# Optimization experiments

Hardware: AMD Instinct MI355X
Metric: run time of the kernel (lower is better)

The kernel has to match this reference:

```python
import jax, jax.numpy as jnp
import numpy as np

B, C, Hh, Ww = 64, 128, 28, 28   # batch, channels, subband H, subband W (H/2, W/2 of input)
NB, BS = 4, 32                    # num_blocks, block_size (C = NB*BS)
ORI = 6                           # DTCWT orientation subbands


def setup_inputs() -> dict:
    key = jax.random.key(0)
    ks = jax.random.split(key, 7)
    return {
        "xl": jax.random.normal(ks[0], (B, C, Hh, Ww), jnp.float32),
        "xh": jax.random.normal(ks[1], (B, C, ORI, Hh, Ww, 2), jnp.float32),
        "w_ll": jax.random.normal(ks[2], (C, Hh, Ww), jnp.float32) * 0.02,
        "w1": jax.random.normal(ks[3], (2, NB, BS, BS), jnp.float32) * 0.02,
        "w2": jax.random.normal(ks[4], (2, NB, BS, BS), jnp.float32) * 0.02,
        "b1": jax.random.normal(ks[5], (2, NB, BS), jnp.float32) * 0.02,
        "b2": jax.random.normal(ks[6], (2, NB, BS), jnp.float32) * 0.02,
    }


def _mul(x, w):
    # block-diagonal matmul: x [..., nb, bs_in], w [nb, bs_in, bs_out]
    return jnp.einsum('...bd,bdk->...bk', x, w)


def reference(xl, xh, w_ll, w1, w2, b1, b2):
    # lowpass: elementwise weighting (broadcast over batch)
    xl_out = xl * w_ll

    b, c = xh.shape[0], xh.shape[1]
    # (B,C,6,H,W,2) -> (2,B,6,H,W,C) -> (2,B,6,H,W,NB,BS)
    x = jnp.transpose(xh, (5, 0, 2, 3, 4, 1))
    x = x.reshape(2, b, ORI, xh.shape[3], xh.shape[4], NB, BS)
    xr, xi = x[0], x[1]

    # complex block-diagonal layer 1 + ReLU
    r1 = jax.nn.relu(_mul(xr, w1[0]) - _mul(xi, w1[1]) + b1[0])
    i1 = jax.nn.relu(_mul(xr, w1[1]) + _mul(xi, w1[0]) + b1[1])
    # complex block-diagonal layer 2 (linear)
    r2 = _mul(r1, w2[0]) - _mul(i1, w2[1]) + b2[0]
    i2 = _mul(r1, w2[1]) + _mul(i1, w2[0]) + b2[1]

    # stack real/imag last, merge blocks back to C, restore (B,C,6,H,W,2)
    out = jnp.stack([r2, i2], axis=-1)                               # (B,6,H,W,NB,BS,2)
    out = out.reshape(b, ORI, xh.shape[3], xh.shape[4], NB * BS, 2)  # (B,6,H,W,C,2)
    xh_out = jnp.transpose(out, (0, 4, 1, 2, 3, 5))                  # (B,C,6,H,W,2)
    # softshrink lambd == 0.0 -> identity (the torch code skips it)
    return xl_out, xh_out
```

## Files before the change

### kernel.cpp

```cpp
#include <hip/hip_runtime.h>

typedef __bf16 bf16x8 __attribute__((ext_vector_type(8)));
typedef float  f32x4  __attribute__((ext_vector_type(4)));


static __device__ __forceinline__ unsigned short bf16bits(float f) {
  __bf16 h = (__bf16)f;
  return __builtin_bit_cast(unsigned short, h);
}

__global__ void prep_weights(const float* __restrict__ w1, const float* __restrict__ w2,
                             unsigned short* __restrict__ wg) {
  const int e = blockIdx.x * 256 + threadIdx.x;
  const int nb    = e >> 13;
  const int layer = (e >> 12) & 1;
  const int n = (e >> 6) & 63;
  const int k = e & 63;
  const float* w = layer ? w2 : w1;
  const int kk = k & 31, nn = n & 31;
  float v;
  if (n < 32) {
    v = (k < 32) ?  w[((0 * 4 + nb) * 32 + kk) * 32 + nn]
                 : -w[((1 * 4 + nb) * 32 + kk) * 32 + nn];
  } else {
    v = (k < 32) ?  w[((1 * 4 + nb) * 32 + kk) * 32 + nn]
                 :  w[((0 * 4 + nb) * 32 + kk) * 32 + nn];
  }
  wg[e] = bf16bits(v);
}

__global__ void ll_kernel(const float* __restrict__ xl, const float* __restrict__ wll,
                          float* __restrict__ out) {
  const int i = blockIdx.x * 256 + threadIdx.x;
  const float4 x = reinterpret_cast<const float4*>(xl)[i];
  const float4 w = reinterpret_cast<const float4*>(wll)[i % 25088];
  float4 o;
  o.x = x.x * w.x; o.y = x.y * w.y; o.z = x.z * w.z; o.w = x.w * w.w;
  reinterpret_cast<float4*>(out)[i] = o;
}

__global__ __launch_bounds__(256, 3)
void xh_kernel(const float* __restrict__ xh, const unsigned short* __restrict__ wg,
               const float* __restrict__ b1, const float* __restrict__ b2,
               float* __restrict__ oxh) {
  __shared__ __align__(16) unsigned short Xs[256 * 64];
  __shared__ __align__(16) unsigned short Ws[2 * 64 * 64];
  __shared__ __align__(16) float Bs[128];

  const int t = threadIdx.x;
  const int bi = blockIdx.x;
  const int mt  = bi % 196;
  const int snb = bi / 196;
  const int ori = snb >> 2;
  const int nb  = snb & 3;
  const int p0 = mt << 8;

  if (t < 128) {
    const int layer = t >> 6, n = t & 63;
    const float* bsrc = layer ? b2 : b1;
    Bs[t] = bsrc[((n >> 5) * 4 + nb) * 32 + (n & 31)];
  }

  {
    const unsigned short* wgn = wg + nb * 8192;
#pragma unroll
    for (int it = 0; it < 4; ++it) {
      const int idx = it * 256 + t;
      const int layer = idx >> 9;
      const int n = (idx >> 3) & 63;
      const int g = idx & 7;
      const uint4 v = *reinterpret_cast<const uint4*>(wgn + layer * 4096 + n * 64 + g * 8);
      char* dst = reinterpret_cast<char*>(Ws) + layer * 8192 + n * 128 + ((g ^ ((n >> 1) & 7)) * 16);
      *reinterpret_cast<uint4*>(dst) = v;
    }
  }

  {
    const float* xb = xh + (size_t)(nb * 32) * 9408 + ori * 1568;
#pragma unroll
    for (int it = 0; it < 8; ++it) {
      const int idx = it * 256 + t;
      const int c = (idx >> 7) * 2;
      const int p = (idx & 127) * 2;
      const int P = p0 + p;
      const int bb = P / 784;
      const int hw = P - bb * 784;
      const float* src = xb + (size_t)bb * 1204224 + c * 9408 + hw * 2;
      const float4 vA = *reinterpret_cast<const float4*>(src);
      const float4 vB = *reinterpret_cast<const float4*>(src + 9408);
      const int g0 = c >> 3;
      const int off = (c & 7) * 2;
      const int s0 = (p >> 1) & 7;
      char* base = reinterpret_cast<char*>(Xs);
      *reinterpret_cast<unsigned int*>(base + p * 128 + ((g0 ^ s0) * 16) + off) =
          (unsigned int)bf16bits(vA.x) | ((unsigned int)bf16bits(vB.x) << 16);
      *reinterpret_cast<unsigned int*>(base + p * 128 + (((g0 + 4) ^ s0) * 16) + off) =
          (unsigned int)bf16bits(vA.y) | ((unsigned int)bf16bits(vB.y) << 16);
      *reinterpret_cast<unsigned int*>(base + (p + 1) * 128 + ((g0 ^ s0) * 16) + off) =
          (unsigned int)bf16bits(vA.z) | ((unsigned int)bf16bits(vB.z) << 16);
      *reinterpret_cast<unsigned int*>(base + (p + 1) * 128 + (((g0 + 4) ^ s0) * 16) + off) =
          (unsigned int)bf16bits(vA.w) | ((unsigned int)bf16bits(vB.w) << 16);
    }
  }
  __syncthreads();

  const int lane = t & 63;
  const int wv = t >> 6;
  const int lr = lane & 15;
  const int lg = lane >> 4;

  f32x4 acc[4][4];
#pragma unroll
  for (int mi = 0; mi < 4; ++mi)
#pragma unroll
    for (int ni = 0; ni < 4; ++ni)
      acc[mi][ni] = (f32x4){0.f, 0.f, 0.f, 0.f};

#pragma unroll
  for (int ks = 0; ks < 2; ++ks) {
    bf16x8 wf[4], xf[4];
#pragma unroll
    for (int mi = 0; mi < 4; ++mi) {
      const int n = mi * 16 + lr;
      wf[mi] = *reinterpret_cast<const bf16x8*>(reinterpret_cast<const char*>(Ws)
                 + n * 128 + (((ks * 4 + lg) ^ ((n >> 1) & 7)) * 16));
    }
#pragma unroll
    for (int ni = 0; ni < 4; ++ni) {
      const int p = wv * 64 + ni * 16 + lr;
      xf[ni] = *reinterpret_cast<const bf16x8*>(reinterpret_cast<const char*>(Xs)
                 + p * 128 + (((ks * 4 + lg) ^ ((p >> 1) & 7)) * 16));
    }
#pragma unroll
    for (int mi = 0; mi < 4; ++mi)
#pragma unroll
      for (int ni = 0; ni < 4; ++ni)
        acc[mi][ni] = __builtin_amdgcn_mfma_f32_16x16x32_bf16(wf[mi], xf[ni], acc[mi][ni], 0, 0, 0);
  }

#pragma unroll
  for (int mi = 0; mi < 4; ++mi) {
    const f32x4 bv = *reinterpret_cast<const f32x4*>(&Bs[mi * 16 + lg * 4]);
    const int gH = mi * 2 + (lg >> 1);
    const int offH = (lg & 1) * 8;
#pragma unroll
    for (int ni = 0; ni < 4; ++ni) {
      const int p = wv * 64 + ni * 16 + lr;
      const float h0 = fmaxf(acc[mi][ni][0] + bv[0], 0.f);
      const float h1 = fmaxf(acc[mi][ni][1] + bv[1], 0.f);
      const float h2 = fmaxf(acc[mi][ni][2] + bv[2], 0.f);
      const float h3 = fmaxf(acc[mi][ni][3] + bv[3], 0.f);
      uint2 u;
      u.x = (unsigned int)bf16bits(h0) | ((unsigned int)bf16bits(h1) << 16);
      u.y = (unsigned int)bf16bits(h2) | ((unsigned int)bf16bits(h3) << 16);
      char* dst = reinterpret_cast<char*>(Xs) + p * 128 + ((gH ^ ((p >> 1) & 7)) * 16) + offH;
      *reinterpret_cast<uint2*>(dst) = u;
    }
  }
  __syncthreads();

  f32x4 acc2[4][4];
#pragma unroll
  for (int mi = 0; mi < 4; ++mi)
#pragma unroll
    for (int ni = 0; ni < 4; ++ni)
      acc2[mi][ni] = (f32x4){0.f, 0.f, 0.f, 0.f};

#pragma unroll
  for (int ks = 0; ks < 2; ++ks) {
    bf16x8 wf[4], hf[4];
#pragma unroll
    for (int mi = 0; mi < 4; ++mi) {
      const int n = mi * 16 + lr;
      wf[mi] = *reinterpret_cast<const bf16x8*>(reinterpret_cast<const char*>(Ws)
                 + 8192 + n * 128 + (((ks * 4 + lg) ^ ((n >> 1) & 7)) * 16));
    }
#pragma unroll
    for (int ni = 0; ni < 4; ++ni) {
      const int p = wv * 64 + ni * 16 + lr;
      hf[ni] = *reinterpret_cast<const bf16x8*>(reinterpret_cast<const char*>(Xs)
                 + p * 128 + (((ks * 4 + lg) ^ ((p >> 1) & 7)) * 16));
    }
#pragma unroll
    for (int mi = 0; mi < 4; ++mi)
#pragma unroll
      for (int ni = 0; ni < 4; ++ni)
        acc2[mi][ni] = __builtin_amdgcn_mfma_f32_16x16x32_bf16(wf[mi], hf[ni], acc2[mi][ni], 0, 0, 0);
  }

  float* ob = oxh + (size_t)(nb * 32) * 9408 + ori * 1568;
#pragma unroll
  for (int ni = 0; ni < 4; ++ni) {
    const int p = wv * 64 + ni * 16 + lr;
    const int P = p0 + p;
    const int bb = P / 784;
    const int hw = P - bb * 784;
    float* obase = ob + (size_t)bb * 1204224 + hw * 2;
#pragma unroll
    for (int mi = 0; mi < 2; ++mi) {
      const f32x4 bre = *reinterpret_cast<const f32x4*>(&Bs[64 + mi * 16 + lg * 4]);
      const f32x4 bim = *reinterpret_cast<const f32x4*>(&Bs[64 + (mi + 2) * 16 + lg * 4]);
#pragma unroll
      for (int j = 0; j < 4; ++j) {
        const int c = mi * 16 + lg * 4 + j;
        float2 v;
        v.x = acc2[mi][ni][j] + bre[j];
        v.y = acc2[mi + 2][ni][j] + bim[j];
        *reinterpret_cast<float2*>(obase + (size_t)c * 9408) = v;
      }
    }
  }
}

extern "C" void kernel_launch(void* const* d_in, const int* in_sizes, int n_in,
                              void* d_out, int out_size, void* d_ws, size_t ws_size,
                              hipStream_t stream) {
  (void)in_sizes; (void)n_in; (void)out_size; (void)ws_size;
  const float* xl  = (const float*)d_in[0];
  const float* xh  = (const float*)d_in[1];
  const float* wll = (const float*)d_in[2];
  const float* w1  = (const float*)d_in[3];
  const float* w2  = (const float*)d_in[4];
  const float* b1  = (const float*)d_in[5];
  const float* b2  = (const float*)d_in[6];
  float* out = (float*)d_out;
  unsigned short* wg = (unsigned short*)d_ws;

  prep_weights<<<128, 256, 0, stream>>>(w1, w2, wg);
  ll_kernel<<<6272, 256, 0, stream>>>(xl, wll, out);
  xh_kernel<<<6 * 4 * 196, 256, 0, stream>>>(xh, wg, b1, b2, out + 6422528);
}
```

Measured before the change: 150.3 us.

## Fuse lowpass into xh kernel, process four tiles per block with register prefetch

Merges the lowpass elementwise kernel into the main kernel, with every fourth block doing lowpass work. Each xh block now handles four 256-pixel tiles and prefetches the next tile's global loads into registers while computing the current one. Weights are pre-swizzled in the prep kernel so the shared-memory copy is a straight copy. This cuts launch count and exposed load latency, but uses more registers and fewer blocks, and the lowpass blocks are mixed in with MFMA blocks.

```diff
diff --git a/kernel.cpp b/kernel.cpp
--- a/kernel.cpp
+++ b/kernel.cpp
@@ -5,8 +5,10 @@
 
 
 static __device__ __forceinline__ unsigned short bf16bits(float f) {
-  __bf16 h = (__bf16)f;
-  return __builtin_bit_cast(unsigned short, h);
+  __bf16 h = (__bf16)f; return __builtin_bit_cast(unsigned short, h);
+}
+static __device__ __forceinline__ unsigned int pack2(float a, float b) {
+  return (unsigned int)bf16bits(a) | ((unsigned int)bf16bits(b) << 16);
 }
 
 __global__ void prep_weights(const float* __restrict__ w1, const float* __restrict__ w2,
@@ -26,187 +28,206 @@
     v = (k < 32) ?  w[((1 * 4 + nb) * 32 + kk) * 32 + nn]
                  :  w[((0 * 4 + nb) * 32 + kk) * 32 + nn];
   }
-  wg[e] = bf16bits(v);
-}
-
-__global__ void ll_kernel(const float* __restrict__ xl, const float* __restrict__ wll,
-                          float* __restrict__ out) {
-  const int i = blockIdx.x * 256 + threadIdx.x;
-  const float4 x = reinterpret_cast<const float4*>(xl)[i];
-  const float4 w = reinterpret_cast<const float4*>(wll)[i % 25088];
-  float4 o;
-  o.x = x.x * w.x; o.y = x.y * w.y; o.z = x.z * w.z; o.w = x.w * w.w;
-  reinterpret_cast<float4*>(out)[i] = o;
+  const int pos = nb * 8192 + layer * 4096 + n * 64 + (((k >> 3) ^ ((n >> 1) & 7)) * 8) + (k & 7);
+  wg[pos] = bf16bits(v);
 }
 
 __global__ __launch_bounds__(256, 3)
-void xh_kernel(const float* __restrict__ xh, const unsigned short* __restrict__ wg,
-               const float* __restrict__ b1, const float* __restrict__ b2,
-               float* __restrict__ oxh) {
+void fused_kernel(const float* __restrict__ xh, const unsigned short* __restrict__ wg,
+                  const float* __restrict__ b1, const float* __restrict__ b2,
+                  const float* __restrict__ xl, const float* __restrict__ wll,
+                  float* __restrict__ out) {
   __shared__ __align__(16) unsigned short Xs[256 * 64];
   __shared__ __align__(16) unsigned short Ws[2 * 64 * 64];
   __shared__ __align__(16) float Bs[128];
 
   const int t = threadIdx.x;
   const int bi = blockIdx.x;
-  const int mt  = bi % 196;
-  const int snb = bi / 196;
+
+  if ((bi & 3) == 3) {
+    const int llb = bi >> 2;
+    const float4* xi4 = reinterpret_cast<const float4*>(xl);
+    const float4* w4  = reinterpret_cast<const float4*>(wll);
+    float4* o4 = reinterpret_cast<float4*>(out);
+#pragma unroll
+    for (int j = 0; j < 16; ++j) {
+      const int i = llb * 4096 + j * 256 + t;
+      const float4 x = xi4[i];
+      const float4 w = w4[i % 25088];
+      float4 r; r.x = x.x * w.x; r.y = x.y * w.y; r.z = x.z * w.z; r.w = x.w * w.w;
+      o4[i] = r;
+    }
+    return;
+  }
+
+  const int xi = (bi >> 2) * 3 + (bi & 3);
+  const int tb  = xi % 49;
+  const int snb = xi / 49;
   const int ori = snb >> 2;
   const int nb  = snb & 3;
-  const int p0 = mt << 8;
+  const int p00 = tb << 10;
 
   if (t < 128) {
     const int layer = t >> 6, n = t & 63;
     const float* bsrc = layer ? b2 : b1;
     Bs[t] = bsrc[((n >> 5) * 4 + nb) * 32 + (n & 31)];
   }
-
   {
-    const unsigned short* wgn = wg + nb * 8192;
-#pragma unroll
-    for (int it = 0; it < 4; ++it) {
-      const int idx = it * 256 + t;
-      const int layer = idx >> 9;
-      const int n = (idx >> 3) & 63;
-      const int g = idx & 7;
-      const uint4 v = *reinterpret_cast<const uint4*>(wgn + layer * 4096 + n * 64 + g * 8);
-      char* dst = reinterpret_cast<char*>(Ws) + layer * 8192 + n * 128 + ((g ^ ((n >> 1) & 7)) * 16);
-      *reinterpret_cast<uint4*>(dst) = v;
-    }
-  }
-
-  {
-    const float* xb = xh + (size_t)(nb * 32) * 9408 + ori * 1568;
-#pragma unroll
-    for (int it = 0; it < 8; ++it) {
-      const int idx = it * 256 + t;
+    const uint4* src = reinterpret_cast<const uint4*>(wg + nb * 8192);
+    uint4* dst = reinterpret_cast<uint4*>(Ws);
+#pragma unroll
+    for (int it = 0; it < 4; ++it) dst[it * 256 + t] = src[it * 256 + t];
+  }
+
+  const int lane = t & 63;
+  const int wv = t >> 6;
+  const int lr = lane & 15;
+  const int lg = lane >> 4;
+  const float* xb = xh + (size_t)(nb * 32) * 9408 + ori * 1568;
+  float* ob = out + 6422528 + (size_t)(nb * 32) * 9408 + ori * 1568;
+  char* XB = reinterpret_cast<char*>(Xs);
+  const char* WB = reinterpret_cast<const char*>(Ws);
+
+  f32x4 R[16];
+
+  auto issue_loads = [&](int p0) {
+#pragma unroll
+    for (int j = 0; j < 8; ++j) {
+      const int idx = j * 256 + t;
       const int c = (idx >> 7) * 2;
       const int p = (idx & 127) * 2;
       const int P = p0 + p;
       const int bb = P / 784;
       const int hw = P - bb * 784;
-      const float* src = xb + (size_t)bb * 1204224 + c * 9408 + hw * 2;
-      const float4 vA = *reinterpret_cast<const float4*>(src);
-      const float4 vB = *reinterpret_cast<const float4*>(src + 9408);
+      const float* s = xb + (size_t)bb * 1204224 + c * 9408 + hw * 2;
+      R[2 * j]     = *reinterpret_cast<const f32x4*>(s);
+      R[2 * j + 1] = *reinterpret_cast<const f32x4*>(s + 9408);
+    }
+  };
+  auto stage_writes = [&]() {
+#pragma unroll
+    for (int j = 0; j < 8; ++j) {
+      const int idx = j * 256 + t;
+      const int c = (idx >> 7) * 2;
+      const int p = (idx & 127) * 2;
       const int g0 = c >> 3;
       const int off = (c & 7) * 2;
       const int s0 = (p >> 1) & 7;
-      char* base = reinterpret_cast<char*>(Xs);
-      *reinterpret_cast<unsigned int*>(base + p * 128 + ((g0 ^ s0) * 16) + off) =
-          (unsigned int)bf16bits(vA.x) | ((unsigned int)bf16bits(vB.x) << 16);
-      *reinterpret_cast<unsigned int*>(base + p * 128 + (((g0 + 4) ^ s0) * 16) + off) =
-          (unsigned int)bf16bits(vA.y) | ((unsigned int)bf16bits(vB.y) << 16);
-      *reinterpret_cast<unsigned int*>(base + (p + 1) * 128 + ((g0 ^ s0) * 16) + off) =
-          (unsigned int)bf16bits(vA.z) | ((unsigned int)bf16bits(vB.z) << 16);
-      *reinterpret_cast<unsigned int*>(base + (p + 1) * 128 + (((g0 + 4) ^ s0) * 16) + off) =
-          (unsigned int)bf16bits(vA.w) | ((unsigned int)bf16bits(vB.w) << 16);
-    }
-  }
+      const f32x4 vA = R[2 * j], vB = R[2 * j + 1];
+      *reinterpret_cast<unsigned int*>(XB + p * 128 + ((g0 ^ s0) * 16) + off)             = pack2(vA[0], vB[0]);
+      *reinterpret_cast<unsigned int*>(XB + p * 128 + (((g0 + 4) ^ s0) * 16) + off)       = pack2(vA[1], vB[1]);
+      *reinterpret_cast<unsigned int*>(XB + (p + 1) * 128 + ((g0 ^ s0) * 16) + off)       = pack2(vA[2], vB[2]);
+      *reinterpret_cast<unsigned int*>(XB + (p + 1) * 128 + (((g0 + 4) ^ s0) * 16) + off) = pack2(vA[3], vB[3]);
+    }
+  };
+
+  issue_loads(p00);
+  stage_writes();
   __syncthreads();
-
-  const int lane = t & 63;
-  const int wv = t >> 6;
-  const int lr = lane & 15;
-  const int lg = lane >> 4;
-
-  f32x4 acc[4][4];
-#pragma unroll
-  for (int mi = 0; mi < 4; ++mi)
-#pragma unroll
-    for (int ni = 0; ni < 4; ++ni)
-      acc[mi][ni] = (f32x4){0.f, 0.f, 0.f, 0.f};
-
-#pragma unroll
-  for (int ks = 0; ks < 2; ++ks) {
-    bf16x8 wf[4], xf[4];
+  issue_loads(p00 + 256);
+
+#pragma unroll
+  for (int tt = 0; tt < 4; ++tt) {
+    f32x4 acc[4][4];
+#pragma unroll
+    for (int mi = 0; mi < 4; ++mi)
+#pragma unroll
+      for (int ni = 0; ni < 4; ++ni)
+        acc[mi][ni] = (f32x4){0.f, 0.f, 0.f, 0.f};
+
+#pragma unroll
+    for (int ks = 0; ks < 2; ++ks) {
+      bf16x8 wf[4], xf[4];
+#pragma unroll
+      for (int mi = 0; mi < 4; ++mi) {
+        const int n = mi * 16 + lr;
+        wf[mi] = *reinterpret_cast<const bf16x8*>(WB + n * 128 + (((ks * 4 + lg) ^ ((n >> 1) & 7)) * 16));
+      }
+#pragma unroll
+      for (int ni = 0; ni < 4; ++ni) {
+        const int p = wv * 64 + ni * 16 + lr;
+        xf[ni] = *reinterpret_cast<const bf16x8*>(XB + p * 128 + (((ks * 4 + lg) ^ ((p >> 1) & 7)) * 16));
+      }
+#pragma unroll
+      for (int mi = 0; mi < 4; ++mi)
+#pragma unroll
+        for (int ni = 0; ni < 4; ++ni)
+          acc[mi][ni] = __builtin_amdgcn_mfma_f32_16x16x32_bf16(wf[mi], xf[ni], acc[mi][ni], 0, 0, 0);
+    }
+
 #pragma unroll
     for (int mi = 0; mi < 4; ++mi) {
-      const int n = mi * 16 + lr;
-      wf[mi] = *reinterpret_cast<const bf16x8*>(reinterpret_cast<const char*>(Ws)
-                 + n * 128 + (((ks * 4 + lg) ^ ((n >> 1) & 7)) * 16));
-    }
-#pragma unroll
-    for (int ni = 0; ni < 4; ++ni) {
-      const int p = wv * 64 + ni * 16 + lr;
-      xf[ni] = *reinterpret_cast<const bf16x8*>(reinterpret_cast<const char*>(Xs)
-                 + p * 128 + (((ks * 4 + lg) ^ ((p >> 1) & 7)) * 16));
-    }
+      const f32x4 bv = *reinterpret_cast<const f32x4*>(&Bs[mi * 16 + lg * 4]);
+      const int gH = mi * 2 + (lg >> 1);
+      const int offH = (lg & 1) * 8;
+#pragma unroll
+      for (int ni = 0; ni < 4; ++ni) {
+        const int p = wv * 64 + ni * 16 + lr;
+        const float h0 = fmaxf(acc[mi][ni][0] + bv[0], 0.f);
+        const float h1 = fmaxf(acc[mi][ni][1] + bv[1], 0.f);
+        const float h2 = fmaxf(acc[mi][ni][2] + bv[2], 0.f);
+        const float h3 = fmaxf(acc[mi][ni][3] + bv[3], 0.f);
+        uint2 u; u.x = pack2(h0, h1); u.y = pack2(h2, h3);
+        *reinterpret_cast<uint2*>(XB + p * 128 + ((gH ^ ((p >> 1) & 7)) * 16) + offH) = u;
+      }
+    }
+
+    f32x4 acc2[4][4];
 #pragma unroll
     for (int mi = 0; mi < 4; ++mi)
 #pragma unroll
       for (int ni = 0; ni < 4; ++ni)
-        acc[mi][ni] = __builtin_amdgcn_mfma_f32_16x16x32_bf16(wf[mi], xf[ni], acc[mi][ni], 0, 0, 0);
-  }
-
-#pragma unroll
-  for (int mi = 0; mi < 4; ++mi) {
-    const f32x4 bv = *reinterpret_cast<const f32x4*>(&Bs[mi * 16 + lg * 4]);
-    const int gH = mi * 2 + (lg >> 1);
-    const int offH = (lg & 1) * 8;
-#pragma unroll
-    for (int ni = 0; ni < 4; ++ni) {
-      const int p = wv * 64 + ni * 16 + lr;
-      const float h0 = fmaxf(acc[mi][ni][0] + bv[0], 0.f);
-      const float h1 = fmaxf(acc[mi][ni][1] + bv[1], 0.f);
-      const float h2 = fmaxf(acc[mi][ni][2] + bv[2], 0.f);
-      const float h3 = fmaxf(acc[mi][ni][3] + bv[3], 0.f);
-      uint2 u;
-      u.x = (unsigned int)bf16bits(h0) | ((unsigned int)bf16bits(h1) << 16);
-      u.y = (unsigned int)bf16bits(h2) | ((unsigned int)bf16bits(h3) << 16);
-      char* dst = reinterpret_cast<char*>(Xs) + p * 128 + ((gH ^ ((p >> 1) & 7)) * 16) + offH;
-      *reinterpret_cast<uint2*>(dst) = u;
-    }
-  }
-  __syncthreads();
-
-  f32x4 acc2[4][4];
-#pragma unroll
-  for (int mi = 0; mi < 4; ++mi)
-#pragma unroll
-    for (int ni = 0; ni < 4; ++ni)
-      acc2[mi][ni] = (f32x4){0.f, 0.f, 0.f, 0.f};
-
-#pragma unroll
-  for (int ks = 0; ks < 2; ++ks) {
-    bf16x8 wf[4], hf[4];
-#pragma unroll
-    for (int mi = 0; mi < 4; ++mi) {
-      const int n = mi * 16 + lr;
-      wf[mi] = *reinterpret_cast<const bf16x8*>(reinterpret_cast<const char*>(Ws)
-                 + 8192 + n * 128 + (((ks * 4 + lg) ^ ((n >> 1) & 7)) * 16));
-    }
-#pragma unroll
-    for (int ni = 0; ni < 4; ++ni) {
-      const int p = wv * 64 + ni * 16 + lr;
-      hf[ni] = *reinterpret_cast<const bf16x8*>(reinterpret_cast<const char*>(Xs)
-                 + p * 128 + (((ks * 4 + lg) ^ ((p >> 1) & 7)) * 16));
-    }
-#pragma unroll
-    for (int mi = 0; mi < 4; ++mi)
-#pragma unroll
-      for (int ni = 0; ni < 4; ++ni)
-        acc2[mi][ni] = __builtin_amdgcn_mfma_f32_16x16x32_bf16(wf[mi], hf[ni], acc2[mi][ni], 0, 0, 0);
-  }
-
-  float* ob = oxh + (size_t)(nb * 32) * 9408 + ori * 1568;
-#pragma unroll
-  for (int ni = 0; ni < 4; ++ni) {
-    const int p = wv * 64 + ni * 16 + lr;
-    const int P = p0 + p;
-    const int bb = P / 784;
-    const int hw = P - bb * 784;
-    float* obase = ob + (size_t)bb * 1204224 + hw * 2;
-#pragma unroll
-    for (int mi = 0; mi < 2; ++mi) {
-      const f32x4 bre = *reinterpret_cast<const f32x4*>(&Bs[64 + mi * 16 + lg * 4]);
-      const f32x4 bim = *reinterpret_cast<const f32x4*>(&Bs[64 + (mi + 2) * 16 + lg * 4]);
-#pragma unroll
-      for (int j = 0; j < 4; ++j) {
-        const int c = mi * 16 + lg * 4 + j;
-        float2 v;
-        v.x = acc2[mi][ni][j] + bre[j];
-        v.y = acc2[mi + 2][ni][j] + bim[j];
-        *reinterpret_cast<float2*>(obase + (size_t)c * 9408) = v;
+        acc2[mi][ni] = (f32x4){0.f, 0.f, 0.f, 0.f};
+
+#pragma unroll
+    for (int ks = 0; ks < 2; ++ks) {
+      bf16x8 wf[4], hf[4];
+#pragma unroll
+      for (int mi = 0; mi < 4; ++mi) {
+        const int n = mi * 16 + lr;
+        wf[mi] = *reinterpret_cast<const bf16x8*>(WB + 8192 + n * 128 + (((ks * 4 + lg) ^ ((n >> 1) & 7)) * 16));
+      }
+#pragma unroll
+      for (int ni = 0; ni < 4; ++ni) {
+        const int p = wv * 64 + ni * 16 + lr;
+        hf[ni] = *reinterpret_cast<const bf16x8*>(XB + p * 128 + (((ks * 4 + lg) ^ ((p >> 1) & 7)) * 16));
+      }
+#pragma unroll
+      for (int mi = 0; mi < 4; ++mi)
+#pragma unroll
+        for (int ni = 0; ni < 4; ++ni)
+          acc2[mi][ni] = __builtin_amdgcn_mfma_f32_16x16x32_bf16(wf[mi], hf[ni], acc2[mi][ni], 0, 0, 0);
+    }
+
+    if (tt < 3) {
+      __syncthreads();
+      stage_writes();
+      __syncthreads();
+      if (tt < 2) issue_loads(p00 + (tt + 2) * 256);
+    }
+
+    {
+      const int p0 = p00 + tt * 256;
+#pragma unroll
+      for (int ni = 0; ni < 4; ++ni) {
+        const int p = wv * 64 + ni * 16 + lr;
+        const int P = p0 + p;
+        const int bb = P / 784;
+        const int hw = P - bb * 784;
+        float* obase = ob + (size_t)bb * 1204224 + hw * 2;
+#pragma unroll
+        for (int mi = 0; mi < 2; ++mi) {
+          const f32x4 bre = *reinterpret_cast<const f32x4*>(&Bs[64 + mi * 16 + lg * 4]);
+          const f32x4 bim = *reinterpret_cast<const f32x4*>(&Bs[64 + (mi + 2) * 16 + lg * 4]);
+#pragma unroll
+          for (int j = 0; j < 4; ++j) {
+            const int c = mi * 16 + lg * 4 + j;
+            float2 v;
+            v.x = acc2[mi][ni][j] + bre[j];
+            v.y = acc2[mi + 2][ni][j] + bim[j];
+            *reinterpret_cast<float2*>(obase + (size_t)c * 9408) = v;
+          }
+        }
       }
     }
   }
@@ -227,6 +248,5 @@
   unsigned short* wg = (unsigned short*)d_ws;
 
   prep_weights<<<128, 256, 0, stream>>>(w1, w2, wg);
-  ll_kernel<<<6272, 256, 0, stream>>>(xl, wll, out);
-  xh_kernel<<<6 * 4 * 196, 256, 0, stream>>>(xh, wg, b1, b2, out + 6422528);
-}
+  fused_kernel<<<1568, 256, 0, stream>>>(xh, wg, b1, b2, xl, wll, out);
+}
```

Result: slower. 217.8 us (+45.0%).
